# Kernel optimization log

Hardware: AMD Instinct MI355X
Metric: run time of the kernel (lower is better)

Reference implementation:

```python
import jax, jax.numpy as jnp
import numpy as np

N = 4096
FIN = 4096
LOC = 16
H1, H2, HEADS = 120, 50, 4
H1_PER = H1 // HEADS
FILM_Z = 32
SSDB_H = 60
N_HEMI = N // 2
NEG_SLOPE = 0.1
GATE_BIAS = -2.0
MASK_FILL = -9e15


def leaky(x):
    return jax.nn.leaky_relu(x, negative_slope=NEG_SLOPE)


def gat(x, mask, W, a_src, a_dst, bias, concat):
    # x: (N, Fin), W: (H, Fin, O), a_src/a_dst: (H, O), mask: (N, N) bool
    wh = jnp.einsum('nf,hfo->hno', x, W)            # (H, N, O)
    f1 = jnp.einsum('hno,ho->hn', wh, a_src)        # (H, N)
    f2 = jnp.einsum('hno,ho->hn', wh, a_dst)        # (H, N)
    e = leaky(f1[:, :, None] + f2[:, None, :])      # (H, N, N)
    e = jnp.where(mask[None], e, MASK_FILL)
    alpha = jax.nn.softmax(e, axis=-1)
    out = jnp.einsum('hij,hjo->hio', alpha, wh)     # (H, N, O)
    if concat:
        h, n, o = out.shape
        out2 = out.transpose(1, 0, 2).reshape(n, h * o)
    else:
        out2 = out.mean(axis=0)
    return out2 + bias


def _uni(k, shape, stdv):
    return jax.random.uniform(k, shape, jnp.float32, -stdv, stdv)


def setup_inputs() -> dict:
    key = jax.random.key(0)
    ks = jax.random.split(key, 30)
    s1 = 1.0 / np.sqrt(H1_PER)
    s2 = 1.0 / np.sqrt(H2)
    inp = {
        'x_fc': jax.random.normal(ks[0], (N, FIN), jnp.float32),
        'adj': jax.random.randint(ks[1], (N, N), 0, 2, jnp.int32),
        'l_loc': jax.random.uniform(ks[2], (N, LOC), jnp.float32),
        # gat1
        'W1': _uni(ks[3], (HEADS, FIN, H1_PER), s1),
        'a1s': _uni(ks[4], (HEADS, H1_PER), s1),
        'a1d': _uni(ks[5], (HEADS, H1_PER), s1),
        'b1': _uni(ks[6], (H1,), s1),
        # gat2
        'W2': _uni(ks[7], (1, H1, H2), s2),
        'a2s': _uni(ks[8], (1, H2), s2),
        'a2d': _uni(ks[9], (1, H2), s2),
        'b2': _uni(ks[10], (H2,), s2),
        # classifier (no bias)
        'Wc': _uni(ks[11], (2, H2), s2),
        # FiLM trunk
        'Wl1': _uni(ks[12], (FILM_Z, LOC), 1.0 / np.sqrt(LOC)),
        'bl1': _uni(ks[13], (FILM_Z,), 1.0 / np.sqrt(LOC)),
        'Wl2': _uni(ks[14], (FILM_Z, FILM_Z), 1.0 / np.sqrt(FILM_Z)),
        'bl2': _uni(ks[15], (FILM_Z,), 1.0 / np.sqrt(FILM_Z)),
        'Wg': _uni(ks[16], (H2, FILM_Z), 1.0 / np.sqrt(FILM_Z)),
        'bg': _uni(ks[17], (H2,), 1.0 / np.sqrt(FILM_Z)),
        'Wb': _uni(ks[18], (H2, FILM_Z), 1.0 / np.sqrt(FILM_Z)),
        'bb': _uni(ks[19], (H2,), 1.0 / np.sqrt(FILM_Z)),
        'Wgate': _uni(ks[20], (1, FILM_Z), 1.0 / np.sqrt(FILM_Z)),
        'bgate': jnp.full((1,), GATE_BIAS, jnp.float32),
        # SSDB hemi
        'Ws1': _uni(ks[21], (SSDB_H, N_HEMI), 1.0 / np.sqrt(N_HEMI)),
        'bs1': _uni(ks[22], (SSDB_H,), 1.0 / np.sqrt(N_HEMI)),
        'Ws2': _uni(ks[23], (1, SSDB_H), 1.0 / np.sqrt(SSDB_H)),
        'bs2': _uni(ks[24], (1,), 1.0 / np.sqrt(SSDB_H)),
    }
    return inp


def reference(x_fc, adj, l_loc, W1, a1s, a1d, b1, W2, a2s, a2d, b2, Wc,
              Wl1, bl1, Wl2, bl2, Wg, bg, Wb, bb, Wgate, bgate,
              Ws1, bs1, Ws2, bs2):
    mask = adj > 0
    h = leaky(gat(x_fc, mask, W1, a1s, a1d, b1, concat=True))    # (N, 120)
    h = leaky(gat(h, mask, W2, a2s, a2d, b2, concat=False))      # (N, 50)
    # FiLM conditioning
    z = leaky(l_loc @ Wl1.T + bl1)
    z = leaky(z @ Wl2.T + bl2)
    gamma = z @ Wg.T + bg                                        # (N, 50)
    beta = z @ Wb.T + bb                                         # (N, 50)
    g = jax.nn.sigmoid(z @ Wgate.T + bgate)                      # (N, 1)
    cov = jnp.clip(l_loc[:, -1], 0.0, 1.0)                       # coverage_power = 1.0
    g = g * cov[:, None]
    h_fused = h + g * (gamma * h + beta)
    logits = leaky(h_fused @ Wc.T)                               # (N, 2)
    # hemisphere SSDB bias
    t = logits.T                                                 # (2, N)
    ipsi = t[:, :N_HEMI]
    contra = t[:, N_HEMI:2 * N_HEMI]
    h_i = leaky(ipsi @ Ws1.T + bs1)                              # (2, 60)
    h_c = leaky(contra @ Ws1.T + bs1)
    b_i = leaky(h_i @ Ws2.T + bs2)                               # (2, 1)
    b_c = leaky(h_c @ Ws2.T + bs2)
    b_mid = 0.5 * (b_i + b_c)                                    # (2, 1)
    bias_nodes = jnp.concatenate([
        jnp.broadcast_to(b_i.T, (N_HEMI, 2)),
        jnp.broadcast_to(b_c.T, (N_HEMI, 2)),
    ], axis=0)                                                   # n_mid = 0
    logits = logits + bias_nodes
    bias_avg = b_mid[:, 0]                                       # (2,)
    return logits, bias_avg
```

## Files before the change

### kernel.cpp

```cpp
#include <hip/hip_runtime.h>

#define NN 4096
#define NNP 4128
#define BROW 132
#define HEADS 4
#define H1PER 30
#define H1DIM 120
#define H2DIM 50

typedef short short8_t __attribute__((ext_vector_type(8)));
typedef float f32x4 __attribute__((ext_vector_type(4)));

__device__ __forceinline__ float lrelu(float x) { return x > 0.f ? x : 0.1f * x; }

__device__ __forceinline__ unsigned short bfrne(float x) {
  unsigned u = __float_as_uint(x);
  u += 0x7fffu + ((u >> 16) & 1u);
  return (unsigned short)(u >> 16);
}
__device__ __forceinline__ unsigned bfpk_rne(float lo, float hi) {
  return (unsigned)bfrne(lo) | ((unsigned)bfrne(hi) << 16);
}
__device__ __forceinline__ unsigned bfpk(float lo, float hi) {
  unsigned a = (__float_as_uint(lo) + 0x8000u) >> 16;
  unsigned b = (__float_as_uint(hi) + 0x8000u) & 0xffff0000u;
  return a | b;
}
__device__ __forceinline__ unsigned fenc(float x) {
  unsigned u = __float_as_uint(x);
  return (u & 0x80000000u) ? ~u : (u | 0x80000000u);
}
__device__ __forceinline__ float fdec(unsigned u) {
  return (u & 0x80000000u) ? __uint_as_float(u ^ 0x80000000u) : __uint_as_float(~u);
}

#define GL16(g, l)                                                                        \
  __builtin_amdgcn_global_load_lds((const __attribute__((address_space(1))) unsigned int*)(g), \
                                   (__attribute__((address_space(3))) unsigned int*)(l), 16, 0, 0)

__global__ __launch_bounds__(256) void k_bits(const int* __restrict__ adj,
                                              unsigned long long* __restrict__ bits,
                                              const float* __restrict__ W1,
                                              const float* __restrict__ a1s,
                                              const float* __restrict__ a1d,
                                              unsigned short* __restrict__ w1t,
                                              unsigned* __restrict__ mxu) {
  int t = threadIdx.x;
  if (blockIdx.x >= 16384) {
    if (blockIdx.x == 16384 && t < 8) mxu[t] = 0;
    int k = (blockIdx.x - 16384) * 256 + t;
#pragma unroll
    for (int h = 0; h < 4; ++h) {
      const float* wp = W1 + ((size_t)h * 4096 + k) * H1PER;
      float fs = 0.f, fd = 0.f;
#pragma unroll
      for (int oo = 0; oo < H1PER; ++oo) {
        float v = wp[oo];
        w1t[(size_t)(h * 30 + oo) * NNP + k] = bfrne(v);
        fs += v * a1s[h * H1PER + oo];
        fd += v * a1d[h * H1PER + oo];
      }
      w1t[(size_t)(120 + h) * NNP + k] = bfrne(fs);
      w1t[(size_t)(124 + h) * NNP + k] = bfrne(fd);
    }
    return;
  }
  int n = blockIdx.x >> 2, r = blockIdx.x & 3;
  size_t base = (size_t)n * 4096 + r * 1024;
  int v0 = adj[base + t];
  int v1 = adj[base + 256 + t];
  int v2 = adj[base + 512 + t];
  int v3 = adj[base + 768 + t];
  unsigned long long m0 = __ballot(v0 > 0);
  unsigned long long m1 = __ballot(v1 > 0);
  unsigned long long m2 = __ballot(v2 > 0);
  unsigned long long m3 = __ballot(v3 > 0);
  if ((t & 63) == 0) {
    size_t w = (size_t)n * (BROW / 2) + r * 16 + (t >> 6);
    bits[w] = m0;
    bits[w + 4] = m1;
    bits[w + 8] = m2;
    bits[w + 12] = m3;
  }
}

__global__ __launch_bounds__(256) void k_gemm1s(const float* __restrict__ x,
                                                const unsigned short* __restrict__ w1t,
                                                float* __restrict__ part) {
  const int t = threadIdx.x;
  const int lane = t & 63, wave = t >> 6;
  const int m = lane & 15, q = lane >> 4;
  const int i0 = blockIdx.x * 128;
  const int kz = blockIdx.y * 512;
  __shared__ float xs[2][128 * 32];
  __shared__ unsigned short bs[2][128 * 32];
  const int ar_ = t >> 3, ac_ = t & 7;
  const float* gxa = x + (size_t)(i0 + ar_) * 4096 + kz + ((ac_ ^ (ar_ & 7)) * 4);
  const int br_ = t >> 2;
  const int bsw = (br_ & 3) ^ ((br_ >> 2) & 3);
  const unsigned short* gwb = w1t + (size_t)br_ * NNP + kz + ((t & 3) ^ bsw) * 8;
  const int asw = m & 7;
  f32x4 acc[2][8];
#pragma unroll
  for (int rg = 0; rg < 2; ++rg)
#pragma unroll
    for (int nt = 0; nt < 8; ++nt) acc[rg][nt] = (f32x4){0.f, 0.f, 0.f, 0.f};

  auto STAGE = [&](int buf, int kk) {
#pragma unroll
    for (int i = 0; i < 4; ++i)
      GL16(gxa + (size_t)i * 32 * 4096 + kk, &xs[buf][(i * 32 + ar_) * 32 + ac_ * 4]);
#pragma unroll
    for (int i = 0; i < 2; ++i)
      GL16(gwb + (size_t)i * 64 * NNP + kk, &bs[buf][(i * 64 + br_) * 32 + (t & 3) * 8]);
  };

  STAGE(0, 0);
#pragma unroll
  for (int it = 0; it < 16; ++it) {
    const int cur = it & 1;
    if (it < 15) {
      STAGE(cur ^ 1, (it + 1) * 32);
      asm volatile("s_waitcnt vmcnt(6)" ::: "memory");
    } else {
      asm volatile("s_waitcnt vmcnt(0)" ::: "memory");
    }
    __builtin_amdgcn_s_barrier();
    __builtin_amdgcn_sched_barrier(0);
    const int c0 = q * 2;
    union { short8_t v; unsigned u[4]; } A[2];
#pragma unroll
    for (int rg = 0; rg < 2; ++rg) {
      const int arow = wave * 32 + rg * 16 + m;
      float4 a0 = *(const float4*)&xs[cur][arow * 32 + ((c0 ^ asw) * 4)];
      float4 a1 = *(const float4*)&xs[cur][arow * 32 + (((c0 + 1) ^ asw) * 4)];
      A[rg].u[0] = bfpk_rne(a0.x, a0.y);
      A[rg].u[1] = bfpk_rne(a0.z, a0.w);
      A[rg].u[2] = bfpk_rne(a1.x, a1.y);
      A[rg].u[3] = bfpk_rne(a1.z, a1.w);
    }
#pragma unroll
    for (int nt = 0; nt < 8; ++nt) {
      const int f = nt * 16 + m;
      const int fsw = (f & 3) ^ ((f >> 2) & 3);
      short8_t B = *(const short8_t*)&bs[cur][f * 32 + ((q ^ fsw) * 8)];
      acc[0][nt] = __builtin_amdgcn_mfma_f32_16x16x32_bf16(A[0].v, B, acc[0][nt], 0, 0, 0);
      acc[1][nt] = __builtin_amdgcn_mfma_f32_16x16x32_bf16(A[1].v, B, acc[1][nt], 0, 0, 0);
    }
    __builtin_amdgcn_sched_barrier(0);
    __builtin_amdgcn_s_barrier();
  }
  float* pp = part + ((size_t)blockIdx.y * 4096 + i0 + wave * 32 + q * 4) * 128 + m;
#pragma unroll
  for (int rg = 0; rg < 2; ++rg)
#pragma unroll
    for (int nt = 0; nt < 8; ++nt)
#pragma unroll
      for (int r = 0; r < 4; ++r) pp[(rg * 16 + r) * 128 + nt * 16] = acc[rg][nt][r];
}

__global__ __launch_bounds__(256) void k_f1c(const float* __restrict__ part,
                                             unsigned short* __restrict__ whbt,
                                             float* __restrict__ f1, float* __restrict__ f2,
                                             unsigned* __restrict__ mxu1) {
  const int t = threadIdx.x;
  const int n = blockIdx.x * 16 + (t >> 4);
  const int og = (t & 15) * 8;
  __shared__ float f2loc[16][4];
  float s[8] = {0.f, 0.f, 0.f, 0.f, 0.f, 0.f, 0.f, 0.f};
  for (int z = 0; z < 8; ++z) {
    const float* pp = part + ((size_t)z * NN + n) * 128 + og;
    float4 u0 = *(const float4*)pp;
    float4 u1 = *(const float4*)(pp + 4);
    s[0] += u0.x; s[1] += u0.y; s[2] += u0.z; s[3] += u0.w;
    s[4] += u1.x; s[5] += u1.y; s[6] += u1.z; s[7] += u1.w;
  }
  if (og < 120) {
#pragma unroll
    for (int j = 0; j < 8; ++j) {
      int o = og + j;
      int h = o / 30, oo = o - h * 30;
      whbt[(size_t)(h * 32 + oo) * NNP + n] = bfrne(s[j]);
    }
  } else {
#pragma unroll
    for (int j = 0; j < 4; ++j) {
      f1[(size_t)j * NN + n] = s[j];
      f2[(size_t)j * NN + n] = s[4 + j];
      f2loc[t >> 4][j] = s[4 + j];
    }
  }
  if ((t & 15) < 8) {
    int h = (t & 15) >> 1, odd = (t & 15) & 1;
    whbt[(size_t)(h * 32 + 30 + odd) * NNP + n] = odd ? 0 : 0x3f80;
  }
  __syncthreads();
  if (t < 4) {
    float m = f2loc[0][t];
#pragma unroll
    for (int i = 1; i < 16; ++i) m = fmaxf(m, f2loc[i][t]);
    atomicMax(&mxu1[t], fenc(m));
  }
}

__global__ __launch_bounds__(256) void k_att1m(const unsigned short* __restrict__ whbt,
                                               const float* __restrict__ f1, const float* __restrict__ f2,
                                               const unsigned* __restrict__ mxu1,
                                               const unsigned int* __restrict__ bits32,
                                               float* __restrict__ part) {
  const int h = blockIdx.y, js = blockIdx.z;
  const int t = threadIdx.x;
  const int lane = t & 63, wave = t >> 6;
  const int m = lane & 15, q = lane >> 4;
  const int i0w = blockIdx.x * 128 + wave * 32;
  const int jbase = js * 1024;
  const float mxh = fdec(mxu1[h]);
  __shared__ float2 es[1024];
  __shared__ unsigned short bsm1[2][8192];
  for (int e = t; e < 1024; e += 256) {
    float fv = f2[h * NN + jbase + e] - mxh;
    es[e] = make_float2(__expf(fv), __expf(0.1f * fv));
  }
  float Rr[2];
  const uint4* br[2];
#pragma unroll
  for (int rg = 0; rg < 2; ++rg) {
    const float f1r = f1[h * NN + i0w + rg * 16 + m];
    const float s = f1r + mxh;
    Rr[rg] = __expf(fminf(60.f, -0.9f * s));
    br[rg] = (const uint4*)(bits32 + (size_t)(i0w + rg * 16 + m) * BROW + (jbase >> 5));
  }
  const float2* fp = es;
  const int r_st = t >> 3;
  const unsigned short* gB = whbt + (size_t)(h * 32 + r_st) * NNP + jbase + ((t & 7) ^ (r_st & 7)) * 8;
  f32x4 acc[2][2];
#pragma unroll
  for (int rg = 0; rg < 2; ++rg) {
    acc[rg][0] = (f32x4){0.f, 0.f, 0.f, 0.f};
    acc[rg][1] = (f32x4){0.f, 0.f, 0.f, 0.f};
  }

  __syncthreads();

#pragma unroll
  for (int c = 0; c < 4; ++c) GL16(gB + c * 64, &bsm1[0][c * 2048 + t * 8]);

#pragma unroll
  for (int jc = 0; jc < 4; ++jc) {
    const int cur = jc & 1;
    uint4 bqq[2][2];
#pragma unroll
    for (int rg = 0; rg < 2; ++rg) {
      bqq[rg][0] = br[rg][jc * 2];
      bqq[rg][1] = br[rg][jc * 2 + 1];
    }
    if (jc < 3) {
#pragma unroll
      for (int c = 0; c < 4; ++c) GL16(gB + (jc + 1) * 256 + c * 64, &bsm1[cur ^ 1][c * 2048 + t * 8]);
      asm volatile("s_waitcnt vmcnt(4)" ::: "memory");
    } else {
      asm volatile("s_waitcnt vmcnt(0)" ::: "memory");
    }
    __builtin_amdgcn_s_barrier();
    __builtin_amdgcn_sched_barrier(0);
#pragma unroll
    for (int g = 0; g < 2; ++g) {
#pragma unroll
      for (int sub = 0; sub < 4; ++sub) {
        const int jl = (jc * 2 + g) * 128 + sub * 32;
        float4 e01 = *(const float4*)(fp + jl + q * 8);
        float4 e23 = *(const float4*)(fp + jl + q * 8 + 2);
        float4 e45 = *(const float4*)(fp + jl + q * 8 + 4);
        float4 e67 = *(const float4*)(fp + jl + q * 8 + 6);
        const int p = g * 16 + sub * 4 + q;
        short8_t b0 = *(const short8_t*)&bsm1[cur][(p >> 3) * 2048 + m * 64 + ((p & 7) ^ (m & 7)) * 8];
        short8_t b1 = *(const short8_t*)&bsm1[cur][(p >> 3) * 2048 + (m + 16) * 64 + ((p & 7) ^ ((m + 16) & 7)) * 8];
#pragma unroll
        for (int rg = 0; rg < 2; ++rg) {
          const uint4 bq = bqq[rg][g];
          unsigned bsel = (sub == 0 ? bq.x : sub == 1 ? bq.y : sub == 2 ? bq.z : bq.w) >> (q * 8);
          const float R = Rr[rg];
          auto sc = [&](float ep, float en, int jj) {
            float wv = fmaxf(ep, R * en);
            return ((bsel >> jj) & 1u) ? wv : 0.f;
          };
          union { short8_t v; unsigned u[4]; } A;
          A.u[0] = bfpk(sc(e01.x, e01.y, 0), sc(e01.z, e01.w, 1));
          A.u[1] = bfpk(sc(e23.x, e23.y, 2), sc(e23.z, e23.w, 3));
          A.u[2] = bfpk(sc(e45.x, e45.y, 4), sc(e45.z, e45.w, 5));
          A.u[3] = bfpk(sc(e67.x, e67.y, 6), sc(e67.z, e67.w, 7));
          acc[rg][0] = __builtin_amdgcn_mfma_f32_16x16x32_bf16(A.v, b0, acc[rg][0], 0, 0, 0);
          acc[rg][1] = __builtin_amdgcn_mfma_f32_16x16x32_bf16(A.v, b1, acc[rg][1], 0, 0, 0);
        }
      }
    }
    __builtin_amdgcn_sched_barrier(0);
    __builtin_amdgcn_s_barrier();
  }
#pragma unroll
  for (int rg = 0; rg < 2; ++rg) {
    float* pp = part + ((size_t)(js * 4 + h) * NN + i0w + rg * 16 + q * 4) * 32 + m;
#pragma unroll
    for (int r = 0; r < 4; ++r) {
      pp[r * 32] = acc[rg][0][r];
      pp[r * 32 + 16] = acc[rg][1][r];
    }
  }
}

__global__ __launch_bounds__(256) void k_fuseA(const float* __restrict__ part, const float* __restrict__ b1,
                                               const float* __restrict__ W2, const float* __restrict__ a2s,
                                               const float* __restrict__ a2d,
                                               unsigned short* __restrict__ whbt2,
                                               float* __restrict__ f1b, float* __restrict__ f2b,
                                               unsigned* __restrict__ mxu2) {
  const int t = threadIdx.x;
  __shared__ float W2s[H1DIM * H2DIM];
  __shared__ float h1s[4][124];
  __shared__ float f2red[4];
  for (int e = t; e < H1DIM * H2DIM; e += 256) W2s[e] = W2[e];
  const int wv = t >> 6, lane = t & 63;
  const int n = blockIdx.x * 4 + wv;
  const int h = lane >> 4, o2 = (lane & 15) * 2;
  float tot0 = 0.f, tot1 = 0.f;
#pragma unroll
  for (int z = 0; z < 4; ++z) {
    const float* pp = part + ((size_t)(z * 4 + h) * NN + n) * 32 + o2;
    float2 u = *(const float2*)pp;
    tot0 += u.x;
    tot1 += u.y;
  }
  float l = __shfl(tot0, h * 16 + 15);
  float inv = 1.f / l;
  if (o2 < 30) {
    h1s[wv][h * 30 + o2] = lrelu(tot0 * inv + b1[h * 30 + o2]);
    h1s[wv][h * 30 + o2 + 1] = lrelu(tot1 * inv + b1[h * 30 + o2 + 1]);
  }
  __syncthreads();
  const int o = lane;
  float acc = 0.f;
  if (o < H2DIM) {
    const float* hr = h1s[wv];
#pragma unroll 4
    for (int k = 0; k < H1DIM; ++k) acc += hr[k] * W2s[k * H2DIM + o];
  }
  unsigned short wbv = (o < H2DIM) ? bfrne(acc) : (o == H2DIM ? (unsigned short)0x3f80 : (unsigned short)0);
  whbt2[(size_t)o * NNP + n] = wbv;
  float ps = (o < H2DIM) ? acc * a2s[o] : 0.f;
  float pd = (o < H2DIM) ? acc * a2d[o] : 0.f;
  for (int off = 32; off > 0; off >>= 1) {
    ps += __shfl_down(ps, off);
    pd += __shfl_down(pd, off);
  }
  if (lane == 0) {
    f1b[n] = ps;
    f2b[n] = pd;
    f2red[wv] = pd;
  }
  __syncthreads();
  if (t == 0) {
    float m = fmaxf(fmaxf(f2red[0], f2red[1]), fmaxf(f2red[2], f2red[3]));
    atomicMax(mxu2, fenc(m));
  }
}

__global__ __launch_bounds__(256) void k_att2m(const unsigned short* __restrict__ whbt2,
                                               const float* __restrict__ f1b, const float* __restrict__ f2b,
                                               const unsigned* __restrict__ mxu2,
                                               const unsigned int* __restrict__ bits32,
                                               float* __restrict__ part) {
  const int js = blockIdx.y;
  const int t = threadIdx.x;
  const int lane = t & 63, wave = t >> 6;
  const int m = lane & 15, q = lane >> 4;
  const int i0w = blockIdx.x * 128 + wave * 32;
  const int jbase = js * 512;
  const float mx0 = fdec(mxu2[0]);
  __shared__ float2 es[512];
  __shared__ unsigned short bsm2[2][8192];
  for (int e = t; e < 512; e += 256) {
    float fv = f2b[jbase + e] - mx0;
    es[e] = make_float2(__expf(fv), __expf(0.1f * fv));
  }
  float Rr[2];
  const uint4* br[2];
#pragma unroll
  for (int rg = 0; rg < 2; ++rg) {
    const float f1r = f1b[i0w + rg * 16 + m];
    const float s = f1r + mx0;
    Rr[rg] = __expf(fminf(60.f, -0.9f * s));
    br[rg] = (const uint4*)(bits32 + (size_t)(i0w + rg * 16 + m) * BROW + (jbase >> 5));
  }
  const float2* fp = es;
  const int r2 = t >> 2;
  const int sw2 = (r2 & 3) ^ ((r2 >> 2) & 3);
  const unsigned short* gB2 = whbt2 + (size_t)r2 * NNP + jbase + ((t & 3) ^ sw2) * 8;
  f32x4 acc[2][4];
#pragma unroll
  for (int rg = 0; rg < 2; ++rg)
#pragma unroll
    for (int xx = 0; xx < 4; ++xx) acc[rg][xx] = (f32x4){0.f, 0.f, 0.f, 0.f};

  __syncthreads();

#pragma unroll
  for (int c = 0; c < 4; ++c) GL16(gB2 + c * 32, &bsm2[0][c * 2048 + t * 8]);

#pragma unroll
  for (int jc = 0; jc < 4; ++jc) {
    const int cur = jc & 1;
    uint4 bqr[2];
    bqr[0] = br[0][jc];
    bqr[1] = br[1][jc];
    if (jc < 3) {
#pragma unroll
      for (int c = 0; c < 4; ++c) GL16(gB2 + (jc + 1) * 128 + c * 32, &bsm2[cur ^ 1][c * 2048 + t * 8]);
      asm volatile("s_waitcnt vmcnt(4)" ::: "memory");
    } else {
      asm volatile("s_waitcnt vmcnt(0)" ::: "memory");
    }
    __builtin_amdgcn_s_barrier();
    __builtin_amdgcn_sched_barrier(0);
#pragma unroll
    for (int sub = 0; sub < 4; ++sub) {
      const int jl = jc * 128 + sub * 32;
      float4 e01 = *(const float4*)(fp + jl + q * 8);
      float4 e23 = *(const float4*)(fp + jl + q * 8 + 2);
      float4 e45 = *(const float4*)(fp + jl + q * 8 + 4);
      float4 e67 = *(const float4*)(fp + jl + q * 8 + 6);
      const int p = sub * 4 + q;
#pragma unroll
      for (int rg = 0; rg < 2; ++rg) {
        const uint4 bq = bqr[rg];
        unsigned bsel = (sub == 0 ? bq.x : sub == 1 ? bq.y : sub == 2 ? bq.z : bq.w) >> (q * 8);
        const float R = Rr[rg];
        auto sc = [&](float ep, float en, int jj) {
          float wv = fmaxf(ep, R * en);
          return ((bsel >> jj) & 1u) ? wv : 0.f;
        };
        union { short8_t v; unsigned u[4]; } A;
        A.u[0] = bfpk(sc(e01.x, e01.y, 0), sc(e01.z, e01.w, 1));
        A.u[1] = bfpk(sc(e23.x, e23.y, 2), sc(e23.z, e23.w, 3));
        A.u[2] = bfpk(sc(e45.x, e45.y, 4), sc(e45.z, e45.w, 5));
        A.u[3] = bfpk(sc(e67.x, e67.y, 6), sc(e67.z, e67.w, 7));
#pragma unroll
        for (int tile = 0; tile < 4; ++tile) {
          const int f = tile * 16 + m;
          const int sw = (f & 3) ^ ((f >> 2) & 3);
          short8_t b = *(const short8_t*)&bsm2[cur][(p >> 2) * 2048 + f * 32 + (((p & 3) ^ sw)) * 8];
          acc[rg][tile] = __builtin_amdgcn_mfma_f32_16x16x32_bf16(A.v, b, acc[rg][tile], 0, 0, 0);
        }
      }
    }
    __builtin_amdgcn_sched_barrier(0);
    __builtin_amdgcn_s_barrier();
  }
#pragma unroll
  for (int rg = 0; rg < 2; ++rg) {
    float* pp = part + ((size_t)js * NN + i0w + rg * 16 + q * 4) * 64 + m;
#pragma unroll
    for (int tile = 0; tile < 4; ++tile)
#pragma unroll
      for (int r = 0; r < 4; ++r) pp[r * 64 + tile * 16] = acc[rg][tile][r];
  }
}

__global__ __launch_bounds__(256) void k_fuseB(const float* __restrict__ part, const float* __restrict__ b2,
                                               const float* __restrict__ l_loc,
                                               const float* __restrict__ Wl1, const float* __restrict__ bl1,
                                               const float* __restrict__ Wl2, const float* __restrict__ bl2,
                                               const float* __restrict__ Wg, const float* __restrict__ bg,
                                               const float* __restrict__ Wb, const float* __restrict__ bb,
                                               const float* __restrict__ Wgate, const float* __restrict__ bgate,
                                               const float* __restrict__ Wc, float* __restrict__ logits) {
  const int t = threadIdx.x;
  const int wv = t >> 6, lane = t & 63;
  const int n = blockIdx.x * 4 + wv;
  const float* p = part + (size_t)n * 64 + lane;
  float tot = 0.f;
#pragma unroll
  for (int z = 0; z < 8; ++z) tot += p[(size_t)z * NN * 64];
  float l = __shfl(tot, 50);
  float hv = (lane < H2DIM) ? lrelu(tot / l + b2[lane]) : 0.f;
  int r32 = lane & 31;
  float locv = l_loc[n * 16 + (lane & 15)];
  float cov = __shfl(locv, 15);
  cov = fminf(fmaxf(cov, 0.f), 1.f);
  float a1v = bl1[r32];
#pragma unroll
  for (int j = 0; j < 16; ++j) a1v += Wl1[r32 * 16 + j] * __shfl(locv, j);
  float z1 = lrelu(a1v);
  float a2v = bl2[r32];
#pragma unroll
  for (int j = 0; j < 32; ++j) a2v += Wl2[r32 * 32 + j] * __shfl(z1, j);
  float z2 = lrelu(a2v);
  float gs = bgate[0];
  float gam, bet;
  {
    int o = lane < H2DIM ? lane : 0;
    gam = bg[o];
    bet = bb[o];
#pragma unroll
    for (int j = 0; j < 32; ++j) {
      float zj = __shfl(z2, j);
      gs += Wgate[j] * zj;
      gam += Wg[o * 32 + j] * zj;
      bet += Wb[o * 32 + j] * zj;
    }
  }
  float g = cov / (1.f + __expf(-gs));
  float hf = hv + g * (gam * hv + bet);
  int o = lane < H2DIM ? lane : 0;
  float p0 = lane < H2DIM ? hf * Wc[o] : 0.f;
  float p1 = lane < H2DIM ? hf * Wc[H2DIM + o] : 0.f;
  for (int off = 32; off > 0; off >>= 1) {
    p0 += __shfl_down(p0, off);
    p1 += __shfl_down(p1, off);
  }
  if (lane == 0) {
    logits[n * 2 + 0] = lrelu(p0);
    logits[n * 2 + 1] = lrelu(p1);
  }
}

__global__ __launch_bounds__(64) void k_ssdbA(const float* __restrict__ logits,
                                              const float* __restrict__ Ws1, const float* __restrict__ bs1,
                                              const float* __restrict__ Ws2, float* __restrict__ hsum) {
  const int k = blockIdx.x, combo = blockIdx.y;
  const int hemi = combo >> 1, c = combo & 1;
  const int lane = threadIdx.x;
  const float* wr = Ws1 + (size_t)k * 2048;
  const float* lc = logits + (size_t)hemi * 4096 + c;
  float acc = 0.f;
#pragma unroll 4
  for (int i = lane; i < 2048; i += 64) acc += wr[i] * lc[2 * i];
  for (int off = 32; off > 0; off >>= 1) acc += __shfl_down(acc, off);
  if (lane == 0) hsum[combo * 60 + k] = lrelu(acc + bs1[k]) * Ws2[k];
}

__global__ __launch_bounds__(256) void k_finB(const float* __restrict__ hsum,
                                              const float* __restrict__ bs2,
                                              const float* __restrict__ logits,
                                              float* __restrict__ out) {
  __shared__ float Bs[4];
  const int t = threadIdx.x;
  {
    int combo = t >> 6, k = t & 63;
    float v = (k < 60) ? hsum[combo * 60 + k] : 0.f;
    for (int off = 32; off > 0; off >>= 1) v += __shfl_down(v, off);
    if (k == 0) Bs[combo] = lrelu(v + bs2[0]);
  }
  __syncthreads();
  int id = blockIdx.x * 256 + t;
  if (id < 2 * NN) {
    int n = id >> 1, c = id & 1;
    out[id] = logits[id] + Bs[(n < 2048 ? 0 : 2) + c];
  } else if (id < 2 * NN + 2) {
    int c = id - 2 * NN;
    out[id] = 0.5f * (Bs[c] + Bs[2 + c]);
  }
}

#define OFF_BITS 0
#define OFF_W1T 540672
#define OFF_GP 804864
#define OFF_A1P 804864
#define OFF_A2P 804864
#define OFF_WH1BT 4999168
#define OFF_F1A 5263360
#define OFF_F2A 5279744
#define OFF_WH2BT 5296128
#define OFF_F12 5428224
#define OFF_F22 5432320
#define OFF_LOG 5436416
#define OFF_MX 5444608
#define OFF_HS 5444672

extern "C" void kernel_launch(void* const* d_in, const int* in_sizes, int n_in,
                              void* d_out, int out_size, void* d_ws, size_t ws_size,
                              hipStream_t stream) {
  const float* x_fc  = (const float*)d_in[0];
  const int*   adj   = (const int*)d_in[1];
  const float* l_loc = (const float*)d_in[2];
  const float* W1    = (const float*)d_in[3];
  const float* a1s   = (const float*)d_in[4];
  const float* a1d   = (const float*)d_in[5];
  const float* b1    = (const float*)d_in[6];
  const float* W2    = (const float*)d_in[7];
  const float* a2s   = (const float*)d_in[8];
  const float* a2d   = (const float*)d_in[9];
  const float* b2    = (const float*)d_in[10];
  const float* Wc    = (const float*)d_in[11];
  const float* Wl1   = (const float*)d_in[12];
  const float* bl1   = (const float*)d_in[13];
  const float* Wl2   = (const float*)d_in[14];
  const float* bl2   = (const float*)d_in[15];
  const float* Wg    = (const float*)d_in[16];
  const float* bg    = (const float*)d_in[17];
  const float* Wb    = (const float*)d_in[18];
  const float* bb    = (const float*)d_in[19];
  const float* Wgate = (const float*)d_in[20];
  const float* bgate = (const float*)d_in[21];
  const float* Ws1   = (const float*)d_in[22];
  const float* bs1   = (const float*)d_in[23];
  const float* Ws2   = (const float*)d_in[24];
  const float* bs2   = (const float*)d_in[25];
  float* out = (float*)d_out;
  float* w = (float*)d_ws;
  unsigned long long* bits = (unsigned long long*)(w + OFF_BITS);
  const unsigned int* bits32 = (const unsigned int*)bits;
  unsigned short* wh1bt = (unsigned short*)(w + OFF_WH1BT);
  unsigned short* wh2bt = (unsigned short*)(w + OFF_WH2BT);
  unsigned short* w1t = (unsigned short*)(w + OFF_W1T);
  unsigned* mxu = (unsigned*)(w + OFF_MX);

  k_bits<<<16400, 256, 0, stream>>>(adj, bits, W1, a1s, a1d, w1t, mxu);
  k_gemm1s<<<dim3(32, 8), 256, 0, stream>>>(x_fc, w1t, w + OFF_GP);
  k_f1c<<<256, 256, 0, stream>>>(w + OFF_GP, wh1bt, w + OFF_F1A, w + OFF_F2A, mxu);
  k_att1m<<<dim3(32, HEADS, 4), 256, 0, stream>>>(wh1bt, w + OFF_F1A, w + OFF_F2A,
                                                  mxu, bits32, w + OFF_A1P);
  k_fuseA<<<1024, 256, 0, stream>>>(w + OFF_A1P, b1, W2, a2s, a2d, wh2bt,
                                    w + OFF_F12, w + OFF_F22, mxu + 4);
  k_att2m<<<dim3(32, 8), 256, 0, stream>>>(wh2bt, w + OFF_F12, w + OFF_F22,
                                           mxu + 4, bits32, w + OFF_A2P);
  k_fuseB<<<1024, 256, 0, stream>>>(w + OFF_A2P, b2, l_loc, Wl1, bl1, Wl2, bl2,
                                    Wg, bg, Wb, bb, Wgate, bgate, Wc, w + OFF_LOG);
  k_ssdbA<<<dim3(60, 4), 64, 0, stream>>>(w + OFF_LOG, Ws1, bs1, Ws2, w + OFF_HS);
  k_finB<<<33, 256, 0, stream>>>(w + OFF_HS, bs2, w + OFF_LOG, out);
}
```

Before: 300.1 us.

## Overlap adjacency bit-packing with GEMM1 and fuse SSDB reduction into final kernel

The W1 transpose/preprocess becomes its own small kernel, and the adjacency bit-packing blocks are merged into the GEMM1 launch. The memory-bound bit-packing can then run alongside the MFMA GEMM blocks instead of in a separate launch. Separately, the two-kernel SSDB tail is fused into one kernel, dropping a launch and the hsum round-trip. The cost is that each of the 33 final blocks now redundantly recomputes all 60 hidden dot products serially per wave.

```diff
diff --git a/kernel.cpp b/kernel.cpp
--- a/kernel.cpp
+++ b/kernel.cpp
@@ -38,62 +38,63 @@
   __builtin_amdgcn_global_load_lds((const __attribute__((address_space(1))) unsigned int*)(g), \
                                    (__attribute__((address_space(3))) unsigned int*)(l), 16, 0, 0)
 
-__global__ __launch_bounds__(256) void k_bits(const int* __restrict__ adj,
-                                              unsigned long long* __restrict__ bits,
-                                              const float* __restrict__ W1,
-                                              const float* __restrict__ a1s,
-                                              const float* __restrict__ a1d,
-                                              unsigned short* __restrict__ w1t,
-                                              unsigned* __restrict__ mxu) {
+__global__ __launch_bounds__(256) void k_pre(const float* __restrict__ W1,
+                                             const float* __restrict__ a1s,
+                                             const float* __restrict__ a1d,
+                                             unsigned short* __restrict__ w1t,
+                                             unsigned* __restrict__ mxu) {
   int t = threadIdx.x;
-  if (blockIdx.x >= 16384) {
-    if (blockIdx.x == 16384 && t < 8) mxu[t] = 0;
-    int k = (blockIdx.x - 16384) * 256 + t;
-#pragma unroll
-    for (int h = 0; h < 4; ++h) {
-      const float* wp = W1 + ((size_t)h * 4096 + k) * H1PER;
-      float fs = 0.f, fd = 0.f;
-#pragma unroll
-      for (int oo = 0; oo < H1PER; ++oo) {
-        float v = wp[oo];
-        w1t[(size_t)(h * 30 + oo) * NNP + k] = bfrne(v);
-        fs += v * a1s[h * H1PER + oo];
-        fd += v * a1d[h * H1PER + oo];
-      }
-      w1t[(size_t)(120 + h) * NNP + k] = bfrne(fs);
-      w1t[(size_t)(124 + h) * NNP + k] = bfrne(fd);
+  if (blockIdx.x == 0 && t < 8) mxu[t] = 0;
+  int k = blockIdx.x * 256 + t;
+#pragma unroll
+  for (int h = 0; h < 4; ++h) {
+    const float* wp = W1 + ((size_t)h * 4096 + k) * H1PER;
+    float fs = 0.f, fd = 0.f;
+#pragma unroll
+    for (int oo = 0; oo < H1PER; ++oo) {
+      float v = wp[oo];
+      w1t[(size_t)(h * 30 + oo) * NNP + k] = bfrne(v);
+      fs += v * a1s[h * H1PER + oo];
+      fd += v * a1d[h * H1PER + oo];
+    }
+    w1t[(size_t)(120 + h) * NNP + k] = bfrne(fs);
+    w1t[(size_t)(124 + h) * NNP + k] = bfrne(fd);
+  }
+}
+
+__global__ __launch_bounds__(256) void k_gb(const float* __restrict__ x,
+                                            const unsigned short* __restrict__ w1t,
+                                            float* __restrict__ part,
+                                            const int* __restrict__ adj,
+                                            unsigned long long* __restrict__ bits) {
+  const int t = threadIdx.x;
+  __shared__ float xs[2][128 * 32];
+  __shared__ unsigned short bs[2][128 * 32];
+  if (blockIdx.x >= 256) {
+    int id = blockIdx.x - 256;
+    int n = id >> 2, r = id & 3;
+    size_t base = (size_t)n * 4096 + r * 1024;
+    int v0 = adj[base + t];
+    int v1 = adj[base + 256 + t];
+    int v2 = adj[base + 512 + t];
+    int v3 = adj[base + 768 + t];
+    unsigned long long m0 = __ballot(v0 > 0);
+    unsigned long long m1 = __ballot(v1 > 0);
+    unsigned long long m2 = __ballot(v2 > 0);
+    unsigned long long m3 = __ballot(v3 > 0);
+    if ((t & 63) == 0) {
+      size_t w = (size_t)n * (BROW / 2) + r * 16 + (t >> 6);
+      bits[w] = m0;
+      bits[w + 4] = m1;
+      bits[w + 8] = m2;
+      bits[w + 12] = m3;
     }
     return;
   }
-  int n = blockIdx.x >> 2, r = blockIdx.x & 3;
-  size_t base = (size_t)n * 4096 + r * 1024;
-  int v0 = adj[base + t];
-  int v1 = adj[base + 256 + t];
-  int v2 = adj[base + 512 + t];
-  int v3 = adj[base + 768 + t];
-  unsigned long long m0 = __ballot(v0 > 0);
-  unsigned long long m1 = __ballot(v1 > 0);
-  unsigned long long m2 = __ballot(v2 > 0);
-  unsigned long long m3 = __ballot(v3 > 0);
-  if ((t & 63) == 0) {
-    size_t w = (size_t)n * (BROW / 2) + r * 16 + (t >> 6);
-    bits[w] = m0;
-    bits[w + 4] = m1;
-    bits[w + 8] = m2;
-    bits[w + 12] = m3;
-  }
-}
-
-__global__ __launch_bounds__(256) void k_gemm1s(const float* __restrict__ x,
-                                                const unsigned short* __restrict__ w1t,
-                                                float* __restrict__ part) {
-  const int t = threadIdx.x;
   const int lane = t & 63, wave = t >> 6;
   const int m = lane & 15, q = lane >> 4;
-  const int i0 = blockIdx.x * 128;
-  const int kz = blockIdx.y * 512;
-  __shared__ float xs[2][128 * 32];
-  __shared__ unsigned short bs[2][128 * 32];
+  const int i0 = (blockIdx.x & 31) * 128;
+  const int kz = (blockIdx.x >> 5) * 512;
   const int ar_ = t >> 3, ac_ = t & 7;
   const float* gxa = x + (size_t)(i0 + ar_) * 4096 + kz + ((ac_ ^ (ar_ & 7)) * 4);
   const int br_ = t >> 2;
@@ -150,7 +151,7 @@
     __builtin_amdgcn_sched_barrier(0);
     __builtin_amdgcn_s_barrier();
   }
-  float* pp = part + ((size_t)blockIdx.y * 4096 + i0 + wave * 32 + q * 4) * 128 + m;
+  float* pp = part + ((size_t)(blockIdx.x >> 5) * 4096 + i0 + wave * 32 + q * 4) * 128 + m;
 #pragma unroll
   for (int rg = 0; rg < 2; ++rg)
 #pragma unroll
@@ -523,41 +524,33 @@
   }
 }
 
-__global__ __launch_bounds__(64) void k_ssdbA(const float* __restrict__ logits,
-                                              const float* __restrict__ Ws1, const float* __restrict__ bs1,
-                                              const float* __restrict__ Ws2, float* __restrict__ hsum) {
-  const int k = blockIdx.x, combo = blockIdx.y;
-  const int hemi = combo >> 1, c = combo & 1;
-  const int lane = threadIdx.x;
-  const float* wr = Ws1 + (size_t)k * 2048;
-  const float* lc = logits + (size_t)hemi * 4096 + c;
-  float acc = 0.f;
-#pragma unroll 4
-  for (int i = lane; i < 2048; i += 64) acc += wr[i] * lc[2 * i];
-  for (int off = 32; off > 0; off >>= 1) acc += __shfl_down(acc, off);
-  if (lane == 0) hsum[combo * 60 + k] = lrelu(acc + bs1[k]) * Ws2[k];
-}
-
-__global__ __launch_bounds__(256) void k_finB(const float* __restrict__ hsum,
-                                              const float* __restrict__ bs2,
-                                              const float* __restrict__ logits,
-                                              float* __restrict__ out) {
+__global__ __launch_bounds__(256) void k_fin(const float* __restrict__ logits,
+                                             const float* __restrict__ Ws1, const float* __restrict__ bs1,
+                                             const float* __restrict__ Ws2, const float* __restrict__ bs2,
+                                             float* __restrict__ out) {
   __shared__ float Bs[4];
   const int t = threadIdx.x;
-  {
-    int combo = t >> 6, k = t & 63;
-    float v = (k < 60) ? hsum[combo * 60 + k] : 0.f;
-    for (int off = 32; off > 0; off >>= 1) v += __shfl_down(v, off);
-    if (k == 0) Bs[combo] = lrelu(v + bs2[0]);
-  }
+  const int wv = t >> 6, lane = t & 63;
+  const int hemi = wv >> 1, c = wv & 1;
+  const float* lc = logits + (size_t)hemi * 4096 + c;
+  float total = 0.f;
+  for (int k = 0; k < 60; ++k) {
+    const float* wr = Ws1 + (size_t)k * 2048;
+    float acc = 0.f;
+#pragma unroll 4
+    for (int i = lane; i < 2048; i += 64) acc += wr[i] * lc[2 * i];
+    for (int off = 32; off > 0; off >>= 1) acc += __shfl_down(acc, off);
+    if (lane == 0) total += lrelu(acc + bs1[k]) * Ws2[k];
+  }
+  if (lane == 0) Bs[wv] = lrelu(total + bs2[0]);
   __syncthreads();
   int id = blockIdx.x * 256 + t;
   if (id < 2 * NN) {
-    int n = id >> 1, c = id & 1;
-    out[id] = logits[id] + Bs[(n < 2048 ? 0 : 2) + c];
+    int n = id >> 1, cc = id & 1;
+    out[id] = logits[id] + Bs[(n < 2048 ? 0 : 2) + cc];
   } else if (id < 2 * NN + 2) {
-    int c = id - 2 * NN;
-    out[id] = 0.5f * (Bs[c] + Bs[2 + c]);
+    int cc = id - 2 * NN;
+    out[id] = 0.5f * (Bs[cc] + Bs[2 + cc]);
   }
 }
 
@@ -574,7 +567,6 @@
 #define OFF_F22 5432320
 #define OFF_LOG 5436416
 #define OFF_MX 5444608
-#define OFF_HS 5444672
 
 extern "C" void kernel_launch(void* const* d_in, const int* in_sizes, int n_in,
                               void* d_out, int out_size, void* d_ws, size_t ws_size,
@@ -614,8 +606,8 @@
   unsigned short* w1t = (unsigned short*)(w + OFF_W1T);
   unsigned* mxu = (unsigned*)(w + OFF_MX);
 
-  k_bits<<<16400, 256, 0, stream>>>(adj, bits, W1, a1s, a1d, w1t, mxu);
-  k_gemm1s<<<dim3(32, 8), 256, 0, stream>>>(x_fc, w1t, w + OFF_GP);
+  k_pre<<<16, 256, 0, stream>>>(W1, a1s, a1d, w1t, mxu);
+  k_gb<<<16640, 256, 0, stream>>>(x_fc, w1t, w + OFF_GP, adj, bits);
   k_f1c<<<256, 256, 0, stream>>>(w + OFF_GP, wh1bt, w + OFF_F1A, w + OFF_F2A, mxu);
   k_att1m<<<dim3(32, HEADS, 4), 256, 0, stream>>>(wh1bt, w + OFF_F1A, w + OFF_F2A,
                                                   mxu, bits32, w + OFF_A1P);
@@ -625,6 +617,5 @@
                                            mxu + 4, bits32, w + OFF_A2P);
   k_fuseB<<<1024, 256, 0, stream>>>(w + OFF_A2P, b2, l_loc, Wl1, bl1, Wl2, bl2,
                                     Wg, bg, Wb, bb, Wgate, bgate, Wc, w + OFF_LOG);
-  k_ssdbA<<<dim3(60, 4), 64, 0, stream>>>(w + OFF_LOG, Ws1, bs1, Ws2, w + OFF_HS);
-  k_finB<<<33, 256, 0, stream>>>(w + OFF_HS, bs2, w + OFF_LOG, out);
-}
+  k_fin<<<33, 256, 0, stream>>>(w + OFF_LOG, Ws1, bs1, Ws2, bs2, out);
+}
```

Result: slower. 490.0 us (+63.3%).
